# Performance work log

Measured on AMD Instinct MI355X. Metric: run time of the kernel, lower is better.

## Reference

```python
import jax, jax.numpy as jnp
import numpy as np

B, D, H, O, E = 65536, 128, 256, 8, 8  # batch, input_dim, hidden_dim, output_dim, n_phases


def setup_inputs() -> dict:
    key = jax.random.key(0)
    ks = jax.random.split(key, 6)
    scale = 0.05
    x = jax.random.normal(ks[0], (B, D), dtype=jnp.float32)
    phases = jax.random.randint(ks[1], (B,), 0, E, dtype=jnp.int32)
    Ws = jax.random.normal(ks[2], (D, H), dtype=jnp.float32) * scale  # shared Linear weight (transposed)
    bs = jnp.zeros((H,), dtype=jnp.float32)
    W1 = jax.random.normal(ks[3], (E, H, H), dtype=jnp.float32) * scale  # per-head first Linear
    b1 = jnp.zeros((E, H), dtype=jnp.float32)
    W2 = jax.random.normal(ks[4], (E, H, O), dtype=jnp.float32) * scale  # per-head second Linear
    b2 = jnp.zeros((E, O), dtype=jnp.float32)
    return {"x": x, "phases": phases, "Ws": Ws, "bs": bs,
            "W1": W1, "b1": b1, "W2": W2, "b2": b2}


def reference(x, phases, Ws, bs, W1, b1, W2, b2):
    # shared trunk: Linear + ReLU
    h = jax.nn.relu(x @ Ws + bs)                                # [B, H]
    # run every head on every sample (dense grouped GEMM), then gather the
    # per-sample routed head. NOTE: no activation between the two head Linears,
    # matching nn.Sequential(Linear, Linear) in the source.
    h1 = jnp.einsum('bh,ehk->ebk', h, W1) + b1[:, None, :]      # [E, B, H]
    y = jnp.einsum('ebk,eko->ebo', h1, W2) + b2[:, None, :]     # [E, B, O]
    q = y[phases, jnp.arange(x.shape[0])]                       # [B, O] routed select
    return q
```

## Files before the change

### kernel.cpp

```cpp
#include <hip/hip_runtime.h>
#include <hip/hip_bf16.h>
#include <cstdint>


using bf16x8 = __attribute__((ext_vector_type(8))) __bf16;
using f32x4  = __attribute__((ext_vector_type(4))) float;

__device__ __forceinline__ unsigned short bf16b(float f) {
    __bf16 h = (__bf16)f;
    return __builtin_bit_cast(unsigned short, h);
}
__device__ __forceinline__ unsigned pack2(float a, float b) {
    return (unsigned)bf16b(a) | ((unsigned)bf16b(b) << 16);
}

__global__ void prep_kernel(const float* __restrict__ Ws,
                            const float* __restrict__ b1,
                            const float* __restrict__ W1,
                            const float* __restrict__ W2,
                            const float* __restrict__ b2,
                            uint4* __restrict__ wsP,
                            unsigned short* __restrict__ wfP,
                            float* __restrict__ bfuse) {
    const int bid = blockIdx.x, tid = threadIdx.x;
    if (bid < 256) {
        __shared__ float w2sT[8][256];
        const int e = bid >> 5, mc = bid & 31;
        const float* W2e = W2 + (size_t)e * 2048;
        #pragma unroll
        for (int h = 0; h < 2; ++h) {
            int f4 = h * 256 + tid;
            float4 v = ((const float4*)W2e)[f4];
            int k = f4 >> 1, o4 = (f4 & 1) * 4;
            w2sT[o4 + 0][k] = v.x;
            w2sT[o4 + 1][k] = v.y;
            w2sT[o4 + 2][k] = v.z;
            w2sT[o4 + 3][k] = v.w;
        }
        __syncthreads();
        const int mloc = tid >> 5, kg = tid & 31;
        const int m = mc * 8 + mloc;
        const float* w1row = W1 + ((size_t)e * 256 + m) * 256;
        float w1v[8];
        #pragma unroll
        for (int i = 0; i < 8; ++i) w1v[i] = w1row[kg + i * 32];
        float acc[8] = {0,0,0,0,0,0,0,0};
        #pragma unroll
        for (int i = 0; i < 8; ++i) {
            int k = kg + i * 32;
            #pragma unroll
            for (int o = 0; o < 8; ++o) acc[o] += w1v[i] * w2sT[o][k];
        }
        #pragma unroll
        for (int o = 0; o < 8; ++o) {
            acc[o] += __shfl_xor(acc[o], 1);
            acc[o] += __shfl_xor(acc[o], 2);
            acc[o] += __shfl_xor(acc[o], 4);
            acc[o] += __shfl_xor(acc[o], 8);
            acc[o] += __shfl_xor(acc[o], 16);
        }
        if (kg == 0) {
            const int kgf  = m >> 5;
            const int lhif = (m >> 3) & 3;
            const int j    = m & 7;
            #pragma unroll
            for (int o = 0; o < 8; ++o) {
                int c = e * 8 + o;
                int lanef = lhif * 16 + (c & 15);
                int F = (kgf * 4 + (c >> 4)) * 64 + lanef;
                wfP[(size_t)F * 8 + j] = bf16b(acc[o]);
            }
        }
    } else if (bid < 272) {
        const int b2i = bid - 256;
        const int kg = b2i >> 2, hi = b2i & 3;
        const int wv = tid >> 6, lane = tid & 63;
        const int l15 = lane & 15, lhi = lane >> 4;
        const int n  = wv * 64 + hi * 16 + l15;
        const int k0 = kg * 32 + lhi * 8;
        float w[8];
        #pragma unroll
        for (int j = 0; j < 8; ++j)
            w[j] = Ws[(size_t)(k0 + j) * 256 + n];
        uint4 u;
        u.x = pack2(w[0], w[1]); u.y = pack2(w[2], w[3]);
        u.z = pack2(w[4], w[5]); u.w = pack2(w[6], w[7]);
        wsP[((kg * 4 + hi) * 4 + wv) * 64 + lane] = u;
    } else {
        const int e = tid >> 5, l = tid & 31;
        float acc[8] = {0,0,0,0,0,0,0,0};
        #pragma unroll
        for (int i = 0; i < 8; ++i) {
            int k = l * 8 + i;
            float a = b1[e * 256 + k];
            const float* w2r = W2 + ((size_t)(e * 256 + k)) * 8;
            #pragma unroll
            for (int o = 0; o < 8; ++o) acc[o] += a * w2r[o];
        }
        #pragma unroll
        for (int o = 0; o < 8; ++o) {
            acc[o] += __shfl_xor(acc[o], 1);
            acc[o] += __shfl_xor(acc[o], 2);
            acc[o] += __shfl_xor(acc[o], 4);
            acc[o] += __shfl_xor(acc[o], 8);
            acc[o] += __shfl_xor(acc[o], 16);
        }
        if (l == 0) {
            #pragma unroll
            for (int o = 0; o < 8; ++o)
                bfuse[e * 8 + o] = acc[o] + b2[e * 8 + o];
        }
    }
}

__global__ __launch_bounds__(256, 2) void fused_kernel(
    const float* __restrict__ x,
    const int* __restrict__ phases,
    const float* __restrict__ bs,
    const uint4* __restrict__ wsP,
    const uint4* __restrict__ wfP,
    const float* __restrict__ bfuse,
    float* __restrict__ out) {
    __shared__ __align__(16) char lds[65536];
    char* xs0 = lds;
    char* xs1 = lds + 16384;
    char* hs  = lds + 32768;

    const int tid = threadIdx.x;
    const int lane = tid & 63;
    const int wv = tid >> 6;
    const int l15 = lane & 15;
    const int lhi = lane >> 4;
    const int blk0 = blockIdx.x * 128;

    const float4* xg = (const float4*)x;

    float4 a0[4], d0[4];
    #pragma unroll
    for (int it = 0; it < 4; ++it) {
        int c = it * 256 + tid;
        int row = c >> 4, col8 = c & 15;
        int gi = (blk0 + row) * 32 + col8 * 2;
        a0[it] = xg[gi]; d0[it] = xg[gi + 1];
    }

    bf16x8 wsA[4][4];
    #pragma unroll
    for (int hi = 0; hi < 4; ++hi)
        #pragma unroll
        for (int kg = 0; kg < 4; ++kg)
            wsA[hi][kg] = __builtin_bit_cast(bf16x8,
                wsP[((kg * 4 + hi) * 4 + wv) * 64 + lane]);
    bf16x8 wfB[8];
    #pragma unroll
    for (int kg = 0; kg < 8; ++kg)
        wfB[kg] = __builtin_bit_cast(bf16x8, wfP[(kg * 4 + wv) * 64 + lane]);
    const float bfv = bfuse[wv * 16 + l15];
    const int myE = wv * 2 + (l15 >> 3);
    const int co  = l15 & 7;

    #pragma unroll
    for (int it = 0; it < 4; ++it) {
        int c = it * 256 + tid;
        int row = c >> 4, col8 = c & 15;
        unsigned addr = (unsigned)(row * 256 + col8 * 16);
        addr ^= (unsigned)((row & 7) << 4);
        uint4 u;
        u.x = pack2(a0[it].x, a0[it].y); u.y = pack2(a0[it].z, a0[it].w);
        u.z = pack2(d0[it].x, d0[it].y); u.w = pack2(d0[it].z, d0[it].w);
        *(uint4*)(xs0 + addr) = u;
    }
    __syncthreads();

    float4 a1[4], d1[4];

    #pragma unroll
    for (int t = 0; t < 2; ++t) {
        const char* xs = t ? xs1 : xs0;
        const int row0 = blk0 + t * 64;

        if (t == 0) {
            #pragma unroll
            for (int it = 0; it < 4; ++it) {
                int c = it * 256 + tid;
                int row = c >> 4, col8 = c & 15;
                int gi = (blk0 + 64 + row) * 32 + col8 * 2;
                a1[it] = xg[gi]; d1[it] = xg[gi + 1];
            }
        }

        f32x4 acc1[4][4];
        #pragma unroll
        for (int hi = 0; hi < 4; ++hi)
            #pragma unroll
            for (int bi = 0; bi < 4; ++bi)
                acc1[hi][bi] = (f32x4){0.f, 0.f, 0.f, 0.f};
        #pragma unroll
        for (int kg = 0; kg < 4; ++kg) {
            bf16x8 xb[4];
            #pragma unroll
            for (int bi = 0; bi < 4; ++bi) {
                int b = bi * 16 + l15;
                unsigned addr = (unsigned)(b * 256 + (kg * 32 + lhi * 8) * 2);
                addr ^= (unsigned)((b & 7) << 4);
                xb[bi] = *(const bf16x8*)(xs + addr);
            }
            __builtin_amdgcn_s_setprio(1);
            #pragma unroll
            for (int hi = 0; hi < 4; ++hi)
                #pragma unroll
                for (int bi = 0; bi < 4; ++bi)
                    acc1[hi][bi] = __builtin_amdgcn_mfma_f32_16x16x32_bf16(
                        wsA[hi][kg], xb[bi], acc1[hi][bi], 0, 0, 0);
            __builtin_amdgcn_s_setprio(0);
        }

        if (t == 0) {
            #pragma unroll
            for (int it = 0; it < 4; ++it) {
                int c = it * 256 + tid;
                int row = c >> 4, col8 = c & 15;
                unsigned addr = (unsigned)(row * 256 + col8 * 16);
                addr ^= (unsigned)((row & 7) << 4);
                uint4 u;
                u.x = pack2(a1[it].x, a1[it].y); u.y = pack2(a1[it].z, a1[it].w);
                u.z = pack2(d1[it].x, d1[it].y); u.w = pack2(d1[it].z, d1[it].w);
                *(uint4*)(xs1 + addr) = u;
            }
        }

        f32x4 bsr[4];
        #pragma unroll
        for (int hi = 0; hi < 4; ++hi)
            bsr[hi] = *(const f32x4*)(bs + wv * 64 + hi * 16 + lhi * 4);
        #pragma unroll
        for (int hi = 0; hi < 4; ++hi)
            #pragma unroll
            for (int bi = 0; bi < 4; ++bi) {
                float v0 = acc1[hi][bi][0] + bsr[hi][0]; v0 = v0 > 0.f ? v0 : 0.f;
                float v1 = acc1[hi][bi][1] + bsr[hi][1]; v1 = v1 > 0.f ? v1 : 0.f;
                float v2 = acc1[hi][bi][2] + bsr[hi][2]; v2 = v2 > 0.f ? v2 : 0.f;
                float v3 = acc1[hi][bi][3] + bsr[hi][3]; v3 = v3 > 0.f ? v3 : 0.f;
                uint2 u; u.x = pack2(v0, v1); u.y = pack2(v2, v3);
                int b = bi * 16 + l15;
                int n0 = wv * 64 + hi * 16 + lhi * 4;
                unsigned addr = (unsigned)(b * 512 + n0 * 2);
                addr ^= (unsigned)((b & 7) << 4);
                *(uint2*)(hs + addr) = u;
            }
        __syncthreads();

        f32x4 acc2[4];
        #pragma unroll
        for (int mi = 0; mi < 4; ++mi)
            acc2[mi] = (f32x4){bfv, bfv, bfv, bfv};
        #pragma unroll
        for (int kg = 0; kg < 8; ++kg) {
            bf16x8 ha[4];
            #pragma unroll
            for (int mi = 0; mi < 4; ++mi) {
                int b = mi * 16 + l15;
                unsigned addr = (unsigned)(b * 512 + (kg * 32 + lhi * 8) * 2);
                addr ^= (unsigned)((b & 7) << 4);
                ha[mi] = *(const bf16x8*)(hs + addr);
            }
            __builtin_amdgcn_s_setprio(1);
            #pragma unroll
            for (int mi = 0; mi < 4; ++mi)
                acc2[mi] = __builtin_amdgcn_mfma_f32_16x16x32_bf16(
                    ha[mi], wfB[kg], acc2[mi], 0, 0, 0);
            __builtin_amdgcn_s_setprio(0);
        }

        #pragma unroll
        for (int mi = 0; mi < 4; ++mi)
            #pragma unroll
            for (int r = 0; r < 4; ++r) {
                int b = mi * 16 + lhi * 4 + r;
                int e = phases[row0 + b];
                if (e == myE)
                    out[(size_t)(row0 + b) * 8 + co] = acc2[mi][r];
            }
        if (t == 0) __syncthreads();
    }
}

extern "C" void kernel_launch(void* const* d_in, const int* in_sizes, int n_in,
                              void* d_out, int out_size, void* d_ws, size_t ws_size,
                              hipStream_t stream) {
    const float* x      = (const float*)d_in[0];
    const int*   phases = (const int*)d_in[1];
    const float* Ws     = (const float*)d_in[2];
    const float* bs     = (const float*)d_in[3];
    const float* W1     = (const float*)d_in[4];
    const float* b1     = (const float*)d_in[5];
    const float* W2     = (const float*)d_in[6];
    const float* b2     = (const float*)d_in[7];
    float* out = (float*)d_out;

    uint4*          wsP   = (uint4*)d_ws;
    unsigned short* wfP   = (unsigned short*)((char*)d_ws + 65536);
    float*          bfuse = (float*)((char*)d_ws + 98304);

    prep_kernel<<<273, 256, 0, stream>>>(Ws, b1, W1, W2, b2,
                                         wsP, wfP, bfuse);
    fused_kernel<<<512, 256, 0, stream>>>(
        x, phases, bs, wsP, (const uint4*)wfP, bfuse, out);
}
```

Before: 24.86 us.

## Process one 64-row tile per block and raise occupancy to three blocks

Each block now handles a single 64-row tile instead of two double-buffered tiles. LDS drops from 64KB to 48KB and the grid doubles to 1024 blocks, with launch bounds raised so three blocks fit per CU. Trunk weights are streamed per k-group (prefetch next) instead of all held in registers, and the fused head weights are loaded after the first GEMM, which lowers peak register pressure. The cost is losing the in-block overlap of the next tile's x load and reloading weights for twice as many blocks.

```diff
diff --git a/kernel.cpp b/kernel.cpp
--- a/kernel.cpp
+++ b/kernel.cpp
@@ -113,7 +113,7 @@
     }
 }
 
-__global__ __launch_bounds__(256, 2) void fused_kernel(
+__global__ __launch_bounds__(256, 3) void fused_kernel(
     const float* __restrict__ x,
     const int* __restrict__ phases,
     const float* __restrict__ bs,
@@ -121,17 +121,16 @@
     const uint4* __restrict__ wfP,
     const float* __restrict__ bfuse,
     float* __restrict__ out) {
-    __shared__ __align__(16) char lds[65536];
-    char* xs0 = lds;
-    char* xs1 = lds + 16384;
-    char* hs  = lds + 32768;
+    __shared__ __align__(16) char lds[49152];
+    char* xs = lds;
+    char* hs = lds + 16384;
 
     const int tid = threadIdx.x;
     const int lane = tid & 63;
     const int wv = tid >> 6;
     const int l15 = lane & 15;
     const int lhi = lane >> 4;
-    const int blk0 = blockIdx.x * 128;
+    const int row0 = blockIdx.x * 64;
 
     const float4* xg = (const float4*)x;
 
@@ -140,21 +139,13 @@
     for (int it = 0; it < 4; ++it) {
         int c = it * 256 + tid;
         int row = c >> 4, col8 = c & 15;
-        int gi = (blk0 + row) * 32 + col8 * 2;
+        int gi = (row0 + row) * 32 + col8 * 2;
         a0[it] = xg[gi]; d0[it] = xg[gi + 1];
     }
-
-    bf16x8 wsA[4][4];
-    #pragma unroll
-    for (int hi = 0; hi < 4; ++hi)
-        #pragma unroll
-        for (int kg = 0; kg < 4; ++kg)
-            wsA[hi][kg] = __builtin_bit_cast(bf16x8,
-                wsP[((kg * 4 + hi) * 4 + wv) * 64 + lane]);
-    bf16x8 wfB[8];
-    #pragma unroll
-    for (int kg = 0; kg < 8; ++kg)
-        wfB[kg] = __builtin_bit_cast(bf16x8, wfP[(kg * 4 + wv) * 64 + lane]);
+    f32x4 bsv[4];
+    #pragma unroll
+    for (int hi = 0; hi < 4; ++hi)
+        bsv[hi] = *(const f32x4*)(bs + wv * 64 + hi * 16 + lhi * 4);
     const float bfv = bfuse[wv * 16 + l15];
     const int myE = wv * 2 + (l15 >> 3);
     const int co  = l15 & 7;
@@ -168,121 +159,103 @@
         uint4 u;
         u.x = pack2(a0[it].x, a0[it].y); u.y = pack2(a0[it].z, a0[it].w);
         u.z = pack2(d0[it].x, d0[it].y); u.w = pack2(d0[it].z, d0[it].w);
-        *(uint4*)(xs0 + addr) = u;
+        *(uint4*)(xs + addr) = u;
     }
     __syncthreads();
 
-    float4 a1[4], d1[4];
-
-    #pragma unroll
-    for (int t = 0; t < 2; ++t) {
-        const char* xs = t ? xs1 : xs0;
-        const int row0 = blk0 + t * 64;
-
-        if (t == 0) {
-            #pragma unroll
-            for (int it = 0; it < 4; ++it) {
-                int c = it * 256 + tid;
-                int row = c >> 4, col8 = c & 15;
-                int gi = (blk0 + 64 + row) * 32 + col8 * 2;
-                a1[it] = xg[gi]; d1[it] = xg[gi + 1];
-            }
-        }
-
-        f32x4 acc1[4][4];
+    f32x4 acc1[4][4];
+    #pragma unroll
+    for (int hi = 0; hi < 4; ++hi)
+        #pragma unroll
+        for (int bi = 0; bi < 4; ++bi)
+            acc1[hi][bi] = (f32x4){0.f, 0.f, 0.f, 0.f};
+    bf16x8 wsCur[4];
+    #pragma unroll
+    for (int hi = 0; hi < 4; ++hi)
+        wsCur[hi] = __builtin_bit_cast(bf16x8, wsP[(hi * 4 + wv) * 64 + lane]);
+    #pragma unroll
+    for (int kg = 0; kg < 4; ++kg) {
+        bf16x8 wsNxt[4];
+        if (kg < 3) {
+            #pragma unroll
+            for (int hi = 0; hi < 4; ++hi)
+                wsNxt[hi] = __builtin_bit_cast(bf16x8,
+                    wsP[(((kg + 1) * 4 + hi) * 4 + wv) * 64 + lane]);
+        }
+        bf16x8 xb[4];
+        #pragma unroll
+        for (int bi = 0; bi < 4; ++bi) {
+            int b = bi * 16 + l15;
+            unsigned addr = (unsigned)(b * 256 + (kg * 32 + lhi * 8) * 2);
+            addr ^= (unsigned)((b & 7) << 4);
+            xb[bi] = *(const bf16x8*)(xs + addr);
+        }
+        __builtin_amdgcn_s_setprio(1);
         #pragma unroll
         for (int hi = 0; hi < 4; ++hi)
             #pragma unroll
             for (int bi = 0; bi < 4; ++bi)
-                acc1[hi][bi] = (f32x4){0.f, 0.f, 0.f, 0.f};
-        #pragma unroll
-        for (int kg = 0; kg < 4; ++kg) {
-            bf16x8 xb[4];
-            #pragma unroll
-            for (int bi = 0; bi < 4; ++bi) {
-                int b = bi * 16 + l15;
-                unsigned addr = (unsigned)(b * 256 + (kg * 32 + lhi * 8) * 2);
-                addr ^= (unsigned)((b & 7) << 4);
-                xb[bi] = *(const bf16x8*)(xs + addr);
-            }
-            __builtin_amdgcn_s_setprio(1);
-            #pragma unroll
-            for (int hi = 0; hi < 4; ++hi)
-                #pragma unroll
-                for (int bi = 0; bi < 4; ++bi)
-                    acc1[hi][bi] = __builtin_amdgcn_mfma_f32_16x16x32_bf16(
-                        wsA[hi][kg], xb[bi], acc1[hi][bi], 0, 0, 0);
-            __builtin_amdgcn_s_setprio(0);
-        }
-
-        if (t == 0) {
-            #pragma unroll
-            for (int it = 0; it < 4; ++it) {
-                int c = it * 256 + tid;
-                int row = c >> 4, col8 = c & 15;
-                unsigned addr = (unsigned)(row * 256 + col8 * 16);
-                addr ^= (unsigned)((row & 7) << 4);
-                uint4 u;
-                u.x = pack2(a1[it].x, a1[it].y); u.y = pack2(a1[it].z, a1[it].w);
-                u.z = pack2(d1[it].x, d1[it].y); u.w = pack2(d1[it].z, d1[it].w);
-                *(uint4*)(xs1 + addr) = u;
-            }
-        }
-
-        f32x4 bsr[4];
-        #pragma unroll
-        for (int hi = 0; hi < 4; ++hi)
-            bsr[hi] = *(const f32x4*)(bs + wv * 64 + hi * 16 + lhi * 4);
-        #pragma unroll
-        for (int hi = 0; hi < 4; ++hi)
-            #pragma unroll
-            for (int bi = 0; bi < 4; ++bi) {
-                float v0 = acc1[hi][bi][0] + bsr[hi][0]; v0 = v0 > 0.f ? v0 : 0.f;
-                float v1 = acc1[hi][bi][1] + bsr[hi][1]; v1 = v1 > 0.f ? v1 : 0.f;
-                float v2 = acc1[hi][bi][2] + bsr[hi][2]; v2 = v2 > 0.f ? v2 : 0.f;
-                float v3 = acc1[hi][bi][3] + bsr[hi][3]; v3 = v3 > 0.f ? v3 : 0.f;
-                uint2 u; u.x = pack2(v0, v1); u.y = pack2(v2, v3);
-                int b = bi * 16 + l15;
-                int n0 = wv * 64 + hi * 16 + lhi * 4;
-                unsigned addr = (unsigned)(b * 512 + n0 * 2);
-                addr ^= (unsigned)((b & 7) << 4);
-                *(uint2*)(hs + addr) = u;
-            }
-        __syncthreads();
-
-        f32x4 acc2[4];
+                acc1[hi][bi] = __builtin_amdgcn_mfma_f32_16x16x32_bf16(
+                    wsCur[hi], xb[bi], acc1[hi][bi], 0, 0, 0);
+        __builtin_amdgcn_s_setprio(0);
+        if (kg < 3) {
+            #pragma unroll
+            for (int hi = 0; hi < 4; ++hi) wsCur[hi] = wsNxt[hi];
+        }
+    }
+
+    #pragma unroll
+    for (int hi = 0; hi < 4; ++hi)
+        #pragma unroll
+        for (int bi = 0; bi < 4; ++bi) {
+            float v0 = acc1[hi][bi][0] + bsv[hi][0]; v0 = v0 > 0.f ? v0 : 0.f;
+            float v1 = acc1[hi][bi][1] + bsv[hi][1]; v1 = v1 > 0.f ? v1 : 0.f;
+            float v2 = acc1[hi][bi][2] + bsv[hi][2]; v2 = v2 > 0.f ? v2 : 0.f;
+            float v3 = acc1[hi][bi][3] + bsv[hi][3]; v3 = v3 > 0.f ? v3 : 0.f;
+            uint2 u; u.x = pack2(v0, v1); u.y = pack2(v2, v3);
+            int b = bi * 16 + l15;
+            int n0 = wv * 64 + hi * 16 + lhi * 4;
+            unsigned addr = (unsigned)(b * 512 + n0 * 2);
+            addr ^= (unsigned)((b & 7) << 4);
+            *(uint2*)(hs + addr) = u;
+        }
+    bf16x8 wfB[8];
+    #pragma unroll
+    for (int kg = 0; kg < 8; ++kg)
+        wfB[kg] = __builtin_bit_cast(bf16x8, wfP[(kg * 4 + wv) * 64 + lane]);
+    __syncthreads();
+
+    f32x4 acc2[4];
+    #pragma unroll
+    for (int mi = 0; mi < 4; ++mi)
+        acc2[mi] = (f32x4){bfv, bfv, bfv, bfv};
+    #pragma unroll
+    for (int kg = 0; kg < 8; ++kg) {
+        bf16x8 ha[4];
+        #pragma unroll
+        for (int mi = 0; mi < 4; ++mi) {
+            int b = mi * 16 + l15;
+            unsigned addr = (unsigned)(b * 512 + (kg * 32 + lhi * 8) * 2);
+            addr ^= (unsigned)((b & 7) << 4);
+            ha[mi] = *(const bf16x8*)(hs + addr);
+        }
+        __builtin_amdgcn_s_setprio(1);
         #pragma unroll
         for (int mi = 0; mi < 4; ++mi)
-            acc2[mi] = (f32x4){bfv, bfv, bfv, bfv};
-        #pragma unroll
-        for (int kg = 0; kg < 8; ++kg) {
-            bf16x8 ha[4];
-            #pragma unroll
-            for (int mi = 0; mi < 4; ++mi) {
-                int b = mi * 16 + l15;
-                unsigned addr = (unsigned)(b * 512 + (kg * 32 + lhi * 8) * 2);
-                addr ^= (unsigned)((b & 7) << 4);
-                ha[mi] = *(const bf16x8*)(hs + addr);
-            }
-            __builtin_amdgcn_s_setprio(1);
-            #pragma unroll
-            for (int mi = 0; mi < 4; ++mi)
-                acc2[mi] = __builtin_amdgcn_mfma_f32_16x16x32_bf16(
-                    ha[mi], wfB[kg], acc2[mi], 0, 0, 0);
-            __builtin_amdgcn_s_setprio(0);
-        }
-
-        #pragma unroll
-        for (int mi = 0; mi < 4; ++mi)
-            #pragma unroll
-            for (int r = 0; r < 4; ++r) {
-                int b = mi * 16 + lhi * 4 + r;
-                int e = phases[row0 + b];
-                if (e == myE)
-                    out[(size_t)(row0 + b) * 8 + co] = acc2[mi][r];
-            }
-        if (t == 0) __syncthreads();
-    }
+            acc2[mi] = __builtin_amdgcn_mfma_f32_16x16x32_bf16(
+                ha[mi], wfB[kg], acc2[mi], 0, 0, 0);
+        __builtin_amdgcn_s_setprio(0);
+    }
+
+    #pragma unroll
+    for (int mi = 0; mi < 4; ++mi)
+        #pragma unroll
+        for (int r = 0; r < 4; ++r) {
+            int b = mi * 16 + lhi * 4 + r;
+            int e = phases[row0 + b];
+            if (e == myE)
+                out[(size_t)(row0 + b) * 8 + co] = acc2[mi][r];
+        }
 }
 
 extern "C" void kernel_launch(void* const* d_in, const int* in_sizes, int n_in,
@@ -304,6 +277,6 @@
 
     prep_kernel<<<273, 256, 0, stream>>>(Ws, b1, W1, W2, b2,
                                          wsP, wfP, bfuse);
-    fused_kernel<<<512, 256, 0, stream>>>(
+    fused_kernel<<<1024, 256, 0, stream>>>(
         x, phases, bs, wsP, (const uint4*)wfP, bfuse, out);
 }
```

Result: slower. 26.19 us (+5.3%).

## Merge weight prep and main kernel into one launch with a grid-wide flag

Applied to the files above, without the earlier changes.

Folds the weight-preparation kernel into the main kernel. The first 256 blocks compute the fused bf16 head weights, the trunk weight pack and the fused bias, then bump a global atomic counter. All blocks load their x tiles first and spin on that counter before reading the packed weights. This removes one kernel launch and overlaps the x loads with weight prep. It adds a memset, a spin-wait that depends on all 512 blocks being co-resident, and more registers held per thread because both x tiles are now live at once.

```diff
diff --git a/kernel.cpp b/kernel.cpp
--- a/kernel.cpp
+++ b/kernel.cpp
@@ -2,7 +2,6 @@
 #include <hip/hip_bf16.h>
 #include <cstdint>
 
-
 using bf16x8 = __attribute__((ext_vector_type(8))) __bf16;
 using f32x4  = __attribute__((ext_vector_type(4))) float;
 
@@ -14,17 +13,47 @@
     return (unsigned)bf16b(a) | ((unsigned)bf16b(b) << 16);
 }
 
-__global__ void prep_kernel(const float* __restrict__ Ws,
-                            const float* __restrict__ b1,
-                            const float* __restrict__ W1,
-                            const float* __restrict__ W2,
-                            const float* __restrict__ b2,
-                            uint4* __restrict__ wsP,
-                            unsigned short* __restrict__ wfP,
-                            float* __restrict__ bfuse) {
+__global__ __launch_bounds__(256, 2) void mono_kernel(
+    const float* __restrict__ x,
+    const int* __restrict__ phases,
+    const float* __restrict__ bs,
+    const float* __restrict__ Ws,
+    const float* __restrict__ b1,
+    const float* __restrict__ W1,
+    const float* __restrict__ W2,
+    const float* __restrict__ b2,
+    uint4* __restrict__ wsP,
+    unsigned short* __restrict__ wfP,
+    float* __restrict__ bfuse,
+    unsigned* __restrict__ sync_c,
+    float* __restrict__ out) {
+    __shared__ __align__(16) char lds[65536];
+    char* xs0 = lds;
+    char* xs1 = lds + 16384;
+    char* hs  = lds + 32768;
+
     const int bid = blockIdx.x, tid = threadIdx.x;
+    const int lane = tid & 63;
+    const int wv = tid >> 6;
+    const int l15 = lane & 15;
+    const int lhi = lane >> 4;
+    const int blk0 = bid * 128;
+
+    const float4* xg = (const float4*)x;
+
+    float4 a0[4], d0[4], a1[4], d1[4];
+    #pragma unroll
+    for (int it = 0; it < 4; ++it) {
+        int c = it * 256 + tid;
+        int row = c >> 4, col8 = c & 15;
+        int gi0 = (blk0 + row) * 32 + col8 * 2;
+        a0[it] = xg[gi0]; d0[it] = xg[gi0 + 1];
+        int gi1 = (blk0 + 64 + row) * 32 + col8 * 2;
+        a1[it] = xg[gi1]; d1[it] = xg[gi1 + 1];
+    }
+
     if (bid < 256) {
-        __shared__ float w2sT[8][256];
+        float (*w2sT)[256] = (float (*)[256])hs;
         const int e = bid >> 5, mc = bid & 31;
         const float* W2e = W2 + (size_t)e * 2048;
         #pragma unroll
@@ -71,93 +100,32 @@
                 wfP[(size_t)F * 8 + j] = bf16b(acc[o]);
             }
         }
-    } else if (bid < 272) {
-        const int b2i = bid - 256;
-        const int kg = b2i >> 2, hi = b2i & 3;
-        const int wv = tid >> 6, lane = tid & 63;
-        const int l15 = lane & 15, lhi = lane >> 4;
-        const int n  = wv * 64 + hi * 16 + l15;
-        const int k0 = kg * 32 + lhi * 8;
-        float w[8];
-        #pragma unroll
-        for (int j = 0; j < 8; ++j)
-            w[j] = Ws[(size_t)(k0 + j) * 256 + n];
-        uint4 u;
-        u.x = pack2(w[0], w[1]); u.y = pack2(w[2], w[3]);
-        u.z = pack2(w[4], w[5]); u.w = pack2(w[6], w[7]);
-        wsP[((kg * 4 + hi) * 4 + wv) * 64 + lane] = u;
-    } else {
-        const int e = tid >> 5, l = tid & 31;
-        float acc[8] = {0,0,0,0,0,0,0,0};
-        #pragma unroll
-        for (int i = 0; i < 8; ++i) {
-            int k = l * 8 + i;
-            float a = b1[e * 256 + k];
-            const float* w2r = W2 + ((size_t)(e * 256 + k)) * 8;
-            #pragma unroll
-            for (int o = 0; o < 8; ++o) acc[o] += a * w2r[o];
-        }
-        #pragma unroll
-        for (int o = 0; o < 8; ++o) {
-            acc[o] += __shfl_xor(acc[o], 1);
-            acc[o] += __shfl_xor(acc[o], 2);
-            acc[o] += __shfl_xor(acc[o], 4);
-            acc[o] += __shfl_xor(acc[o], 8);
-            acc[o] += __shfl_xor(acc[o], 16);
-        }
-        if (l == 0) {
-            #pragma unroll
-            for (int o = 0; o < 8; ++o)
-                bfuse[e * 8 + o] = acc[o] + b2[e * 8 + o];
-        }
-    }
-}
-
-__global__ __launch_bounds__(256, 2) void fused_kernel(
-    const float* __restrict__ x,
-    const int* __restrict__ phases,
-    const float* __restrict__ bs,
-    const uint4* __restrict__ wsP,
-    const uint4* __restrict__ wfP,
-    const float* __restrict__ bfuse,
-    float* __restrict__ out) {
-    __shared__ __align__(16) char lds[65536];
-    char* xs0 = lds;
-    char* xs1 = lds + 16384;
-    char* hs  = lds + 32768;
-
-    const int tid = threadIdx.x;
-    const int lane = tid & 63;
-    const int wv = tid >> 6;
-    const int l15 = lane & 15;
-    const int lhi = lane >> 4;
-    const int blk0 = blockIdx.x * 128;
-
-    const float4* xg = (const float4*)x;
-
-    float4 a0[4], d0[4];
-    #pragma unroll
-    for (int it = 0; it < 4; ++it) {
-        int c = it * 256 + tid;
-        int row = c >> 4, col8 = c & 15;
-        int gi = (blk0 + row) * 32 + col8 * 2;
-        a0[it] = xg[gi]; d0[it] = xg[gi + 1];
-    }
-
-    bf16x8 wsA[4][4];
-    #pragma unroll
-    for (int hi = 0; hi < 4; ++hi)
-        #pragma unroll
-        for (int kg = 0; kg < 4; ++kg)
-            wsA[hi][kg] = __builtin_bit_cast(bf16x8,
-                wsP[((kg * 4 + hi) * 4 + wv) * 64 + lane]);
-    bf16x8 wfB[8];
-    #pragma unroll
-    for (int kg = 0; kg < 8; ++kg)
-        wfB[kg] = __builtin_bit_cast(bf16x8, wfP[(kg * 4 + wv) * 64 + lane]);
-    const float bfv = bfuse[wv * 16 + l15];
-    const int myE = wv * 2 + (l15 >> 3);
-    const int co  = l15 & 7;
+        if (bid < 16) {
+            const int kgp = bid >> 2, hip = bid & 3;
+            const int n  = wv * 64 + hip * 16 + l15;
+            const int k0 = kgp * 32 + lhi * 8;
+            float w[8];
+            #pragma unroll
+            for (int j = 0; j < 8; ++j)
+                w[j] = Ws[(size_t)(k0 + j) * 256 + n];
+            uint4 u;
+            u.x = pack2(w[0], w[1]); u.y = pack2(w[2], w[3]);
+            u.z = pack2(w[4], w[5]); u.w = pack2(w[6], w[7]);
+            wsP[((kgp * 4 + hip) * 4 + wv) * 64 + lane] = u;
+        }
+        if (bid == 16 && tid < 64) {
+            const int e2 = tid >> 3, o = tid & 7;
+            float acc2 = b2[e2 * 8 + o];
+            for (int k = 0; k < 256; ++k)
+                acc2 += b1[e2 * 256 + k] * W2[((size_t)(e2 * 256 + k)) * 8 + o];
+            bfuse[e2 * 8 + o] = acc2;
+        }
+        __threadfence();
+        __syncthreads();
+        if (tid == 0)
+            __hip_atomic_fetch_add(sync_c, 1u, __ATOMIC_RELAXED,
+                                   __HIP_MEMORY_SCOPE_AGENT);
+    }
 
     #pragma unroll
     for (int it = 0; it < 4; ++it) {
@@ -169,25 +137,38 @@
         u.x = pack2(a0[it].x, a0[it].y); u.y = pack2(a0[it].z, a0[it].w);
         u.z = pack2(d0[it].x, d0[it].y); u.w = pack2(d0[it].z, d0[it].w);
         *(uint4*)(xs0 + addr) = u;
-    }
-    __syncthreads();
-
-    float4 a1[4], d1[4];
+        uint4 v;
+        v.x = pack2(a1[it].x, a1[it].y); v.y = pack2(a1[it].z, a1[it].w);
+        v.z = pack2(d1[it].x, d1[it].y); v.w = pack2(d1[it].z, d1[it].w);
+        *(uint4*)(xs1 + addr) = v;
+    }
+
+    while (__hip_atomic_load(sync_c, __ATOMIC_RELAXED,
+                             __HIP_MEMORY_SCOPE_AGENT) < 256u)
+        __builtin_amdgcn_s_sleep(8);
+    __threadfence();
+
+    const uint4* wfPq = (const uint4*)wfP;
+    bf16x8 wsA[4][4];
+    #pragma unroll
+    for (int hi = 0; hi < 4; ++hi)
+        #pragma unroll
+        for (int kg = 0; kg < 4; ++kg)
+            wsA[hi][kg] = __builtin_bit_cast(bf16x8,
+                wsP[((kg * 4 + hi) * 4 + wv) * 64 + lane]);
+    bf16x8 wfB[8];
+    #pragma unroll
+    for (int kg = 0; kg < 8; ++kg)
+        wfB[kg] = __builtin_bit_cast(bf16x8, wfPq[(kg * 4 + wv) * 64 + lane]);
+    const float bfv = bfuse[wv * 16 + l15];
+    const int myE = wv * 2 + (l15 >> 3);
+    const int co  = l15 & 7;
 
     #pragma unroll
     for (int t = 0; t < 2; ++t) {
         const char* xs = t ? xs1 : xs0;
         const int row0 = blk0 + t * 64;
-
-        if (t == 0) {
-            #pragma unroll
-            for (int it = 0; it < 4; ++it) {
-                int c = it * 256 + tid;
-                int row = c >> 4, col8 = c & 15;
-                int gi = (blk0 + 64 + row) * 32 + col8 * 2;
-                a1[it] = xg[gi]; d1[it] = xg[gi + 1];
-            }
-        }
+        __syncthreads();
 
         f32x4 acc1[4][4];
         #pragma unroll
@@ -213,20 +194,6 @@
                     acc1[hi][bi] = __builtin_amdgcn_mfma_f32_16x16x32_bf16(
                         wsA[hi][kg], xb[bi], acc1[hi][bi], 0, 0, 0);
             __builtin_amdgcn_s_setprio(0);
-        }
-
-        if (t == 0) {
-            #pragma unroll
-            for (int it = 0; it < 4; ++it) {
-                int c = it * 256 + tid;
-                int row = c >> 4, col8 = c & 15;
-                unsigned addr = (unsigned)(row * 256 + col8 * 16);
-                addr ^= (unsigned)((row & 7) << 4);
-                uint4 u;
-                u.x = pack2(a1[it].x, a1[it].y); u.y = pack2(a1[it].z, a1[it].w);
-                u.z = pack2(d1[it].x, d1[it].y); u.w = pack2(d1[it].z, d1[it].w);
-                *(uint4*)(xs1 + addr) = u;
-            }
         }
 
         f32x4 bsr[4];
@@ -281,7 +248,6 @@
                 if (e == myE)
                     out[(size_t)(row0 + b) * 8 + co] = acc2[mi][r];
             }
-        if (t == 0) __syncthreads();
     }
 }
 
@@ -298,12 +264,12 @@
     const float* b2     = (const float*)d_in[7];
     float* out = (float*)d_out;
 
-    uint4*          wsP   = (uint4*)d_ws;
-    unsigned short* wfP   = (unsigned short*)((char*)d_ws + 65536);
-    float*          bfuse = (float*)((char*)d_ws + 98304);
-
-    prep_kernel<<<273, 256, 0, stream>>>(Ws, b1, W1, W2, b2,
-                                         wsP, wfP, bfuse);
-    fused_kernel<<<512, 256, 0, stream>>>(
-        x, phases, bs, wsP, (const uint4*)wfP, bfuse, out);
-}
+    uint4*          wsP    = (uint4*)d_ws;
+    unsigned short* wfP    = (unsigned short*)((char*)d_ws + 65536);
+    float*          bfuse  = (float*)((char*)d_ws + 98304);
+    unsigned*       sync_c = (unsigned*)((char*)d_ws + 98560);
+
+    hipMemsetAsync((void*)sync_c, 0, 4, stream);
+    mono_kernel<<<512, 256, 0, stream>>>(
+        x, phases, bs, Ws, b1, W1, W2, b2, wsP, wfP, bfuse, sync_c, out);
+}
```

Result: slower. 98.58 us (+296.5%).

## Process four 64-row tiles per block with rolling double-buffered x prefetch

Applied to the files above, without the earlier changes.

The fused kernel now handles 256 rows per block (256 blocks instead of 512) and loops over four 64-row tiles, prefetching each next tile into the alternate LDS buffer. This amortizes the per-block loading of the weight fragments in registers over more rows. The bias load is hoisted out of the loop, and the store of the next x tile to LDS is moved after the h barrier. The prep kernel issues its W2 global loads before the W1 loads so their latencies overlap. The trade-off is fewer blocks (256 on a GPU with roughly that many CUs), which risks lower occupancy and less latency hiding.

```diff
diff --git a/kernel.cpp b/kernel.cpp
--- a/kernel.cpp
+++ b/kernel.cpp
@@ -27,23 +27,23 @@
         __shared__ float w2sT[8][256];
         const int e = bid >> 5, mc = bid & 31;
         const float* W2e = W2 + (size_t)e * 2048;
-        #pragma unroll
-        for (int h = 0; h < 2; ++h) {
-            int f4 = h * 256 + tid;
-            float4 v = ((const float4*)W2e)[f4];
-            int k = f4 >> 1, o4 = (f4 & 1) * 4;
-            w2sT[o4 + 0][k] = v.x;
-            w2sT[o4 + 1][k] = v.y;
-            w2sT[o4 + 2][k] = v.z;
-            w2sT[o4 + 3][k] = v.w;
-        }
-        __syncthreads();
+        float4 v0 = ((const float4*)W2e)[tid];
+        float4 v1 = ((const float4*)W2e)[256 + tid];
         const int mloc = tid >> 5, kg = tid & 31;
         const int m = mc * 8 + mloc;
         const float* w1row = W1 + ((size_t)e * 256 + m) * 256;
         float w1v[8];
         #pragma unroll
         for (int i = 0; i < 8; ++i) w1v[i] = w1row[kg + i * 32];
+        {
+            int f4 = tid, k = f4 >> 1, o4 = (f4 & 1) * 4;
+            w2sT[o4 + 0][k] = v0.x; w2sT[o4 + 1][k] = v0.y;
+            w2sT[o4 + 2][k] = v0.z; w2sT[o4 + 3][k] = v0.w;
+            f4 = 256 + tid; k = f4 >> 1; o4 = (f4 & 1) * 4;
+            w2sT[o4 + 0][k] = v1.x; w2sT[o4 + 1][k] = v1.y;
+            w2sT[o4 + 2][k] = v1.z; w2sT[o4 + 3][k] = v1.w;
+        }
+        __syncthreads();
         float acc[8] = {0,0,0,0,0,0,0,0};
         #pragma unroll
         for (int i = 0; i < 8; ++i) {
@@ -131,7 +131,7 @@
     const int wv = tid >> 6;
     const int l15 = lane & 15;
     const int lhi = lane >> 4;
-    const int blk0 = blockIdx.x * 128;
+    const int blk0 = blockIdx.x * 256;
 
     const float4* xg = (const float4*)x;
 
@@ -143,7 +143,6 @@
         int gi = (blk0 + row) * 32 + col8 * 2;
         a0[it] = xg[gi]; d0[it] = xg[gi + 1];
     }
-
     bf16x8 wsA[4][4];
     #pragma unroll
     for (int hi = 0; hi < 4; ++hi)
@@ -155,6 +154,10 @@
     #pragma unroll
     for (int kg = 0; kg < 8; ++kg)
         wfB[kg] = __builtin_bit_cast(bf16x8, wfP[(kg * 4 + wv) * 64 + lane]);
+    f32x4 bsv[4];
+    #pragma unroll
+    for (int hi = 0; hi < 4; ++hi)
+        bsv[hi] = *(const f32x4*)(bs + wv * 64 + hi * 16 + lhi * 4);
     const float bfv = bfuse[wv * 16 + l15];
     const int myE = wv * 2 + (l15 >> 3);
     const int co  = l15 & 7;
@@ -172,20 +175,21 @@
     }
     __syncthreads();
 
-    float4 a1[4], d1[4];
-
-    #pragma unroll
-    for (int t = 0; t < 2; ++t) {
-        const char* xs = t ? xs1 : xs0;
+    #pragma unroll
+    for (int t = 0; t < 4; ++t) {
+        const char* xs  = (t & 1) ? xs1 : xs0;
+        char*       xsn = (t & 1) ? xs0 : xs1;
         const int row0 = blk0 + t * 64;
 
-        if (t == 0) {
+        float4 pa[4], pd[4];
+        if (t < 3) {
+            int nrow0 = row0 + 64;
             #pragma unroll
             for (int it = 0; it < 4; ++it) {
                 int c = it * 256 + tid;
                 int row = c >> 4, col8 = c & 15;
-                int gi = (blk0 + 64 + row) * 32 + col8 * 2;
-                a1[it] = xg[gi]; d1[it] = xg[gi + 1];
+                int gi = (nrow0 + row) * 32 + col8 * 2;
+                pa[it] = xg[gi]; pd[it] = xg[gi + 1];
             }
         }
 
@@ -215,7 +219,24 @@
             __builtin_amdgcn_s_setprio(0);
         }
 
-        if (t == 0) {
+        #pragma unroll
+        for (int hi = 0; hi < 4; ++hi)
+            #pragma unroll
+            for (int bi = 0; bi < 4; ++bi) {
+                float v0 = acc1[hi][bi][0] + bsv[hi][0]; v0 = v0 > 0.f ? v0 : 0.f;
+                float v1 = acc1[hi][bi][1] + bsv[hi][1]; v1 = v1 > 0.f ? v1 : 0.f;
+                float v2 = acc1[hi][bi][2] + bsv[hi][2]; v2 = v2 > 0.f ? v2 : 0.f;
+                float v3 = acc1[hi][bi][3] + bsv[hi][3]; v3 = v3 > 0.f ? v3 : 0.f;
+                uint2 u; u.x = pack2(v0, v1); u.y = pack2(v2, v3);
+                int b = bi * 16 + l15;
+                int n0 = wv * 64 + hi * 16 + lhi * 4;
+                unsigned addr = (unsigned)(b * 512 + n0 * 2);
+                addr ^= (unsigned)((b & 7) << 4);
+                *(uint2*)(hs + addr) = u;
+            }
+        __syncthreads();
+
+        if (t < 3) {
             #pragma unroll
             for (int it = 0; it < 4; ++it) {
                 int c = it * 256 + tid;
@@ -223,32 +244,11 @@
                 unsigned addr = (unsigned)(row * 256 + col8 * 16);
                 addr ^= (unsigned)((row & 7) << 4);
                 uint4 u;
-                u.x = pack2(a1[it].x, a1[it].y); u.y = pack2(a1[it].z, a1[it].w);
-                u.z = pack2(d1[it].x, d1[it].y); u.w = pack2(d1[it].z, d1[it].w);
-                *(uint4*)(xs1 + addr) = u;
-            }
-        }
-
-        f32x4 bsr[4];
-        #pragma unroll
-        for (int hi = 0; hi < 4; ++hi)
-            bsr[hi] = *(const f32x4*)(bs + wv * 64 + hi * 16 + lhi * 4);
-        #pragma unroll
-        for (int hi = 0; hi < 4; ++hi)
-            #pragma unroll
-            for (int bi = 0; bi < 4; ++bi) {
-                float v0 = acc1[hi][bi][0] + bsr[hi][0]; v0 = v0 > 0.f ? v0 : 0.f;
-                float v1 = acc1[hi][bi][1] + bsr[hi][1]; v1 = v1 > 0.f ? v1 : 0.f;
-                float v2 = acc1[hi][bi][2] + bsr[hi][2]; v2 = v2 > 0.f ? v2 : 0.f;
-                float v3 = acc1[hi][bi][3] + bsr[hi][3]; v3 = v3 > 0.f ? v3 : 0.f;
-                uint2 u; u.x = pack2(v0, v1); u.y = pack2(v2, v3);
-                int b = bi * 16 + l15;
-                int n0 = wv * 64 + hi * 16 + lhi * 4;
-                unsigned addr = (unsigned)(b * 512 + n0 * 2);
-                addr ^= (unsigned)((b & 7) << 4);
-                *(uint2*)(hs + addr) = u;
-            }
-        __syncthreads();
+                u.x = pack2(pa[it].x, pa[it].y); u.y = pack2(pa[it].z, pa[it].w);
+                u.z = pack2(pd[it].x, pd[it].y); u.w = pack2(pd[it].z, pd[it].w);
+                *(uint4*)(xsn + addr) = u;
+            }
+        }
 
         f32x4 acc2[4];
         #pragma unroll
@@ -281,7 +281,7 @@
                 if (e == myE)
                     out[(size_t)(row0 + b) * 8 + co] = acc2[mi][r];
             }
-        if (t == 0) __syncthreads();
+        if (t < 3) __syncthreads();
     }
 }
 
@@ -304,6 +304,6 @@
 
     prep_kernel<<<273, 256, 0, stream>>>(Ws, b1, W1, W2, b2,
                                          wsP, wfP, bfuse);
-    fused_kernel<<<512, 256, 0, stream>>>(
+    fused_kernel<<<256, 256, 0, stream>>>(
         x, phases, bs, wsP, (const uint4*)wfP, bfuse, out);
 }
```

New measurement: 49.39 us. +98.7%, slower.
